# Performance work log

Measured on AMD Instinct MI355X. Metric: run time of the kernel, lower is better.

The kernel has to match this reference:

```python
import jax, jax.numpy as jnp
import numpy as np

N_HYP = 128           # HPARAM.HV_NUM_OF_HYPOTHESES
ZSCORE_THR = 2.0      # HPARAM.PRUN_ZSCORE_THRESHOLD
IN_MASK_MULT = 10.0   # HPARAM.HV_HYPOTHESIS_IN_MASK_MULTIPLIER


def setup_inputs() -> dict:
    key = jax.random.key(0)
    k1, k2 = jax.random.split(key)
    B, H, W = 16, 96, 96
    uv_img = jax.random.normal(k1, (B, 2, H, W), dtype=jnp.float32)
    mask = jnp.ones((B, H, W), dtype=bool)  # all-ones mask: pts == full pixel grid
    # stands in for torch.multinomial pair sampling over mask pixels
    pair_idx = jax.random.randint(k2, (B, N_HYP, 2), 0, H * W)
    return {"uv_img": uv_img, "mask": mask, "pair_idx": pair_idx}


def _hough_voting(uv_img, pair_idx):
    B, _, H, W = uv_img.shape
    Np = H * W
    # pts in torch.where(mask) row-major order for an all-ones mask
    ys, xs = jnp.meshgrid(jnp.arange(H), jnp.arange(W), indexing='ij')
    pts = jnp.stack([ys.ravel(), xs.ravel()], axis=1).astype(uv_img.dtype)  # [Np,2]
    uvT = uv_img.reshape(B, 2, Np).transpose(0, 2, 1)                       # [B,Np,2]

    # --- hypothesis generation (pair gather + batched 2x2 pinverse solve) ---
    pp = pts[pair_idx]                                   # [B,N,2(pair),2(yx)]
    p0, p1 = pp[:, :, 0], pp[:, :, 1]                    # [B,N,2]
    uv0 = jnp.take_along_axis(uvT, pair_idx[:, :, 0][:, :, None], axis=1)  # [B,N,2]
    uv1 = jnp.take_along_axis(uvT, pair_idx[:, :, 1][:, :, None], axis=1)  # [B,N,2]
    A = jnp.stack([uv0, -uv1], axis=-1)                  # [B,N,2,2]
    Bvec = (p1 - p0)[..., None]                          # [B,N,2,1]
    X = jnp.linalg.pinv(A) @ Bvec                        # [B,N,2,1]
    s = X[:, :, 0, :]                                    # [B,N,1] scale along ray 0
    Y = s * uv0 + p0                                     # [B,N,2] intersection points

    # --- z-score outlier pruning with mean replacement ---
    mean = jnp.mean(Y, axis=1)                           # [B,2]
    std = jnp.std(Y, axis=1, ddof=1)                     # torch.std is unbiased
    z = (Y - mean[:, None, :]) / std[:, None, :]
    outl = (z > ZSCORE_THR)
    outl = (outl[..., 0] | outl[..., 1])[..., None]
    Yp = jnp.where(outl, mean[:, None, :], Y)

    # --- pairwise vote weighting over all mask pixels ---
    a = Yp[:, :, None, :] - pts[None, None]              # [B,N,Np,2]
    a = a / jnp.linalg.norm(a, axis=-1, keepdims=True)
    votes = jnp.einsum('bnpk,bpk->bnp', a, uvT) > 0      # direction agreement
    w = jnp.sum(votes, axis=-1).astype(uv_img.dtype)     # [B,N]
    match = jnp.trunc(Yp)[:, :, None, :] == pts[None, None]
    h_in_mask = jnp.sum(match[..., 0] & match[..., 1], axis=-1)
    w = jnp.where(h_in_mask == 1, IN_MASK_MULT, 1.0) * w
    w = w / jnp.sum(w, axis=1, keepdims=True)

    # --- NaN guard + weighted mean, swap (y,x)->(x,y) ---
    is_nan = jnp.isnan(Yp[..., 0]) | jnp.isnan(Yp[..., 1])
    Yp = jnp.nan_to_num(Yp)
    w = jnp.where(is_nan, 0.0, w)
    weighted_mean = jnp.sum(Yp * w[..., None], axis=1)   # [B,2]
    return weighted_mean[:, ::-1]


def reference(uv_img, mask, pair_idx):
    # mask is all-ones by construction; pts are the full pixel grid (see _hough_voting)
    return _hough_voting(uv_img, pair_idx)
```

## Files before the change

### kernel.cpp

```cpp
#include <hip/hip_runtime.h>
#include <math.h>

namespace {

constexpr int BATCH = 16;
constexpr int Ww = 96;
constexpr int NP = 96 * 96;
constexpr int NHYP = 128;
constexpr int HPB = 4;
constexpr int GPB = NHYP / HPB;

__device__ inline void waveSum2D(double& a, double& b) {
#pragma unroll
  for (int o = 32; o >= 1; o >>= 1) {
    a += __shfl_xor(a, o, 64);
    b += __shfl_xor(b, o, 64);
  }
}
__device__ inline double waveSumD(double v) {
#pragma unroll
  for (int o = 32; o >= 1; o >>= 1) v += __shfl_xor(v, o, 64);
  return v;
}

__global__ __launch_bounds__(256, 4)
void vote_kernel(const float* __restrict__ uv, const int* __restrict__ pair,
                 double* __restrict__ partials ) {
  __shared__ double sPy[NHYP], sPx[NHYP];
  __shared__ float sWm[NHYP];
  __shared__ int sNan[NHYP];
  __shared__ double sh1[2][2], sh2[2][2];
  __shared__ unsigned sC[4][HPB];

  const int t = threadIdx.x;
  const int lane = t & 63;
  const int wv = t >> 6;
  const int b = blockIdx.x >> 5;
  const int g = blockIdx.x & (GPB - 1);
  const float* uvb = uv + (size_t)b * 2 * NP;

  float4 pu[3], pv[3];
#pragma unroll
  for (int i = 0; i < 3; ++i) {
    const int p = (i * 256 + t) * 4;
    pu[i] = *(const float4*)(uvb + p);
    pv[i] = *(const float4*)(uvb + NP + p);
  }

  double Yy = 0.0, Yx = 0.0;
  if (t < NHYP) {
    int i0 = pair[(b * NHYP + t) * 2 + 0];
    int i1 = pair[(b * NHYP + t) * 2 + 1];
    double u0 = uvb[i0], v0 = uvb[NP + i0];
    double u1 = uvb[i1], v1 = uvb[NP + i1];
    double y0 = (double)(i0 / Ww), x0 = (double)(i0 % Ww);
    double y1 = (double)(i1 / Ww), x1 = (double)(i1 % Ww);
    double det = u1 * v0 - u0 * v1;
    double s = (u1 * (x1 - x0) - v1 * (y1 - y0)) / det;
    Yy = s * u0 + y0;
    Yx = s * v0 + x0;
  }
  double sy = Yy, sx = Yx;
  waveSum2D(sy, sx);
  if (lane == 0 && wv < 2) { sh1[wv][0] = sy; sh1[wv][1] = sx; }
  __syncthreads();
  const double my = (sh1[0][0] + sh1[1][0]) * (1.0 / NHYP);
  const double mx = (sh1[0][1] + sh1[1][1]) * (1.0 / NHYP);
  const double dy = Yy - my, dx = Yx - mx;
  double qy = dy * dy, qx = dx * dx;
  waveSum2D(qy, qx);
  if (lane == 0 && wv < 2) { sh2[wv][0] = qy; sh2[wv][1] = qx; }
  __syncthreads();
  if (t < NHYP) {
    double vy = (sh2[0][0] + sh2[1][0]) * (1.0 / (NHYP - 1));
    double vx = (sh2[0][1] + sh2[1][1]) * (1.0 / (NHYP - 1));
    bool outl = (dy > 2.0 * sqrt(vy)) || (dx > 2.0 * sqrt(vx));
    double py = outl ? my : Yy;
    double px = outl ? mx : Yx;
    sPy[t] = py;
    sPx[t] = px;
    sWm[t] = (py > -1.0 && py < 96.0 && px > -1.0 && px < 96.0) ? 10.0f : 1.0f;
    sNan[t] = (isnan(py) || isnan(px)) ? 1 : 0;
  }
  __syncthreads();

  const int hb = g * HPB;
  float yy[HPB], yx[HPB];
#pragma unroll
  for (int h = 0; h < HPB; ++h) {
    yy[h] = (float)sPy[hb + h];
    yx[h] = (float)sPx[hb + h];
  }
  unsigned c[HPB] = {0, 0, 0, 0};
#pragma unroll
  for (int it = 0; it < 9; ++it) {
    float4 u4, v4;
    if (it < 3) {
      u4 = pu[it]; v4 = pv[it];
    } else {
      const int p = (it * 256 + t) * 4;
      u4 = *(const float4*)(uvb + p);
      v4 = *(const float4*)(uvb + NP + p);
    }
    const int p = (it * 256 + t) * 4;
    const int yi = p / Ww;
    const float fy = (float)yi;
    const float fx = (float)(p - yi * Ww);
    const float k0 = fy * u4.x + fx * v4.x;
    const float k1 = fy * u4.y + (fx + 1.0f) * v4.y;
    const float k2 = fy * u4.z + (fx + 2.0f) * v4.z;
    const float k3 = fy * u4.w + (fx + 3.0f) * v4.w;
#pragma unroll
    for (int h = 0; h < HPB; ++h) {
      c[h] += __popcll(__ballot(fmaf(yy[h], u4.x, yx[h] * v4.x) > k0));
      c[h] += __popcll(__ballot(fmaf(yy[h], u4.y, yx[h] * v4.y) > k1));
      c[h] += __popcll(__ballot(fmaf(yy[h], u4.z, yx[h] * v4.z) > k2));
      c[h] += __popcll(__ballot(fmaf(yy[h], u4.w, yx[h] * v4.w) > k3));
    }
  }
  if (lane == 0) {
#pragma unroll
    for (int h = 0; h < HPB; ++h) sC[wv][h] = c[h];
  }
  __syncthreads();

  if (t == 0) {
    double wsum = 0.0, ny = 0.0, nx = 0.0;
#pragma unroll
    for (int h = 0; h < HPB; ++h) {
      const int hh = hb + h;
      unsigned cnt = sC[0][h] + sC[1][h] + sC[2][h] + sC[3][h];
      if (!sNan[hh]) {
        double w = (double)cnt * (double)sWm[hh];
        wsum += w;
        ny += sPy[hh] * w;
        nx += sPx[hh] * w;
      }
    }
    double* slot = partials + (size_t)b * 3 * GPB;
    slot[0 * GPB + g] = wsum;
    slot[1 * GPB + g] = ny;
    slot[2 * GPB + g] = nx;
  }
}

__global__ __launch_bounds__(192)
void final_kernel(const double* __restrict__ partials,
                  float* __restrict__ out) {
  __shared__ double sD[3];
  const int t = threadIdx.x;
  const int lane = t & 63;
  const int wv = t >> 6;
  const int b = blockIdx.x;

  double val = (lane < GPB)
                   ? partials[((size_t)b * 3 + wv) * GPB + lane]
                   : 0.0;
  val = waveSumD(val);
  if (lane == 0) sD[wv] = val;
  __syncthreads();
  if (t == 0) {
    double wsum = sD[0];
    out[b * 2 + 0] = (float)(sD[2] / wsum);
    out[b * 2 + 1] = (float)(sD[1] / wsum);
  }
}

}

extern "C" void kernel_launch(void* const* d_in, const int* in_sizes, int n_in,
                              void* d_out, int out_size, void* d_ws, size_t ws_size,
                              hipStream_t stream) {
  const float* uv = (const float*)d_in[0];
  const int* pair = (const int*)d_in[2];
  float* out = (float*)d_out;

  double* partials = (double*)d_ws;

  vote_kernel<<<BATCH * GPB, 256, 0, stream>>>(uv, pair, partials);
  final_kernel<<<BATCH, 192, 0, stream>>>(partials, out);
}
```

Baseline: 17.10 us.

## Use 512-thread blocks with per-lane vote counters and a final shuffle reduction

Doubles the block size to 512 threads, so each thread handles 18 pixels (four float4 iterations plus a float2 tail) instead of 36. Vote counting switches from a ballot plus popcount per comparison to per-lane integer accumulation, followed by one wave shuffle reduction at the end. It also drops the prefetch of the first uv tiles into registers that overlapped with hypothesis generation. The aim is to cut the serial pixel loop and the per-comparison cross-lane instructions, at the cost of more threads per block, extra shuffles at the end, and losing the early load overlap.

```diff
diff --git a/kernel.cpp b/kernel.cpp
--- a/kernel.cpp
+++ b/kernel.cpp
@@ -9,8 +9,16 @@
 constexpr int NHYP = 128;
 constexpr int HPB = 4;
 constexpr int GPB = NHYP / HPB;
+constexpr int THREADS = 512;
 
 __device__ inline void waveSum2D(double& a, double& b) {
+#pragma unroll
+  for (int o = 32; o >= 1; o >>= 1) {
+    a += __shfl_xor(a, o, 64);
+    b += __shfl_xor(b, o, 64);
+  }
+}
+__device__ inline void waveSum2I(int& a, int& b) {
 #pragma unroll
   for (int o = 32; o >= 1; o >>= 1) {
     a += __shfl_xor(a, o, 64);
@@ -23,14 +31,14 @@
   return v;
 }
 
-__global__ __launch_bounds__(256, 4)
+__global__ __launch_bounds__(THREADS, 4)
 void vote_kernel(const float* __restrict__ uv, const int* __restrict__ pair,
                  double* __restrict__ partials ) {
   __shared__ double sPy[NHYP], sPx[NHYP];
   __shared__ float sWm[NHYP];
   __shared__ int sNan[NHYP];
   __shared__ double sh1[2][2], sh2[2][2];
-  __shared__ unsigned sC[4][HPB];
+  __shared__ int sC[8][HPB];
 
   const int t = threadIdx.x;
   const int lane = t & 63;
@@ -38,14 +46,6 @@
   const int b = blockIdx.x >> 5;
   const int g = blockIdx.x & (GPB - 1);
   const float* uvb = uv + (size_t)b * 2 * NP;
-
-  float4 pu[3], pv[3];
-#pragma unroll
-  for (int i = 0; i < 3; ++i) {
-    const int p = (i * 256 + t) * 4;
-    pu[i] = *(const float4*)(uvb + p);
-    pv[i] = *(const float4*)(uvb + NP + p);
-  }
 
   double Yy = 0.0, Yx = 0.0;
   if (t < NHYP) {
@@ -91,18 +91,12 @@
     yy[h] = (float)sPy[hb + h];
     yx[h] = (float)sPx[hb + h];
   }
-  unsigned c[HPB] = {0, 0, 0, 0};
+  int c[HPB] = {0, 0, 0, 0};
 #pragma unroll
-  for (int it = 0; it < 9; ++it) {
-    float4 u4, v4;
-    if (it < 3) {
-      u4 = pu[it]; v4 = pv[it];
-    } else {
-      const int p = (it * 256 + t) * 4;
-      u4 = *(const float4*)(uvb + p);
-      v4 = *(const float4*)(uvb + NP + p);
-    }
-    const int p = (it * 256 + t) * 4;
+  for (int it = 0; it < 4; ++it) {
+    const int p = (it * THREADS + t) * 4;
+    const float4 u4 = *(const float4*)(uvb + p);
+    const float4 v4 = *(const float4*)(uvb + NP + p);
     const int yi = p / Ww;
     const float fy = (float)yi;
     const float fx = (float)(p - yi * Ww);
@@ -112,12 +106,29 @@
     const float k3 = fy * u4.w + (fx + 3.0f) * v4.w;
 #pragma unroll
     for (int h = 0; h < HPB; ++h) {
-      c[h] += __popcll(__ballot(fmaf(yy[h], u4.x, yx[h] * v4.x) > k0));
-      c[h] += __popcll(__ballot(fmaf(yy[h], u4.y, yx[h] * v4.y) > k1));
-      c[h] += __popcll(__ballot(fmaf(yy[h], u4.z, yx[h] * v4.z) > k2));
-      c[h] += __popcll(__ballot(fmaf(yy[h], u4.w, yx[h] * v4.w) > k3));
+      c[h] += (fmaf(yy[h], u4.x, yx[h] * v4.x) > k0) ? 1 : 0;
+      c[h] += (fmaf(yy[h], u4.y, yx[h] * v4.y) > k1) ? 1 : 0;
+      c[h] += (fmaf(yy[h], u4.z, yx[h] * v4.z) > k2) ? 1 : 0;
+      c[h] += (fmaf(yy[h], u4.w, yx[h] * v4.w) > k3) ? 1 : 0;
     }
   }
+  {
+    const int p = 4 * THREADS * 4 + t * 2;
+    const float2 u2 = *(const float2*)(uvb + p);
+    const float2 v2 = *(const float2*)(uvb + NP + p);
+    const int yi = p / Ww;
+    const float fy = (float)yi;
+    const float fx = (float)(p - yi * Ww);
+    const float k0 = fy * u2.x + fx * v2.x;
+    const float k1 = fy * u2.y + (fx + 1.0f) * v2.y;
+#pragma unroll
+    for (int h = 0; h < HPB; ++h) {
+      c[h] += (fmaf(yy[h], u2.x, yx[h] * v2.x) > k0) ? 1 : 0;
+      c[h] += (fmaf(yy[h], u2.y, yx[h] * v2.y) > k1) ? 1 : 0;
+    }
+  }
+  waveSum2I(c[0], c[1]);
+  waveSum2I(c[2], c[3]);
   if (lane == 0) {
 #pragma unroll
     for (int h = 0; h < HPB; ++h) sC[wv][h] = c[h];
@@ -129,7 +140,9 @@
 #pragma unroll
     for (int h = 0; h < HPB; ++h) {
       const int hh = hb + h;
-      unsigned cnt = sC[0][h] + sC[1][h] + sC[2][h] + sC[3][h];
+      int cnt = 0;
+#pragma unroll
+      for (int w8 = 0; w8 < 8; ++w8) cnt += sC[w8][h];
       if (!sNan[hh]) {
         double w = (double)cnt * (double)sWm[hh];
         wsum += w;
@@ -177,6 +190,6 @@
 
   double* partials = (double*)d_ws;
 
-  vote_kernel<<<BATCH * GPB, 256, 0, stream>>>(uv, pair, partials);
+  vote_kernel<<<BATCH * GPB, THREADS, 0, stream>>>(uv, pair, partials);
   final_kernel<<<BATCH, 192, 0, stream>>>(partials, out);
 }
```

New measurement: 14.38 us, median of 2. -15.9%, faster.
